# Performance work log

Measured on AMD Instinct MI355X. Metric: run time of the kernel, lower is better.

Reference implementation:

```python
import jax, jax.numpy as jnp
import numpy as np

B, N, D_IN, H, R = 4096, 32, 256, 256, 3
VIRTUAL_DECAY = 0.7


def setup_inputs() -> dict:
    key = jax.random.key(0)
    ks = jax.random.split(key, 16)
    def xavier(k, shape):
        fan_in, fan_out = shape[-1], shape[-2]
        lim = np.sqrt(6.0 / (fan_in + fan_out))
        return jax.random.uniform(k, shape, jnp.float32, -lim, lim)
    return {
        'input_vec': jax.random.normal(ks[0], (B, D_IN), jnp.float32),
        'child_h': jax.random.normal(ks[1], (B, N, H), jnp.float32),
        'child_c': jax.random.normal(ks[2], (B, N, H), jnp.float32),
        'relation_ids': jax.random.randint(ks[3], (B, N), 0, R, jnp.int32),
        'virtual_mask': jax.random.randint(ks[4], (B, N), 0, 2, jnp.int32).astype(bool),
        'rel_emb': xavier(ks[5], (R, H)),
        'W_i': xavier(ks[6], (H, D_IN + H)), 'b_i': jnp.full((H,), 0.1, jnp.float32),
        'W_f': xavier(ks[7], (R, H, H)),     'b_f': jnp.full((R, H), 0.1, jnp.float32),
        'W_o': xavier(ks[8], (H, D_IN + H)), 'b_o': jnp.full((H,), 0.1, jnp.float32),
        'W_u': xavier(ks[9], (H, D_IN + H)), 'b_u': jnp.full((H,), 0.1, jnp.float32),
        'w_att': xavier(ks[10], (1, H)).reshape(H), 'b_att': jnp.full((1,), 0.1, jnp.float32),
    }


def reference(input_vec, child_h, child_c, relation_ids, virtual_mask,
              rel_emb, W_i, b_i, W_f, b_f, W_o, b_o, W_u, b_u, w_att, b_att):
    # virtual-node decay applied to both child states
    decay = jnp.where(virtual_mask, VIRTUAL_DECAY, 1.0)[..., None]          # (B,N,1)
    ch = child_h * decay                                                     # (B,N,H)
    cc = child_c * decay                                                     # (B,N,H)

    # relation-aware attention over children (softmax over child axis)
    re = rel_emb[relation_ids]                                               # (B,N,H)
    scores = jnp.einsum('bnh,h->bn', re + ch, w_att) + b_att[0]              # (B,N)
    attn = jax.nn.softmax(scores, axis=1)[..., None]                         # (B,N,1)
    child_h_sum = jnp.sum(ch * attn, axis=1)                                 # (B,H)

    # relation-routed forget gates: compute all R linears, gather by relation id
    # NOTE: original applies NO sigmoid to f (faithful to source)
    f_all = jnp.einsum('bnh,rgh->bnrg', ch, W_f) + b_f                       # (B,N,R,H)
    f = jnp.take_along_axis(f_all, relation_ids[:, :, None, None], axis=2)[:, :, 0, :]  # (B,N,H)
    child_c_sum = jnp.sum(f * cc, axis=1)                                    # (B,H)

    combined = jnp.concatenate([input_vec, child_h_sum], axis=-1)            # (B,D_IN+H)
    i = jax.nn.sigmoid(combined @ W_i.T + b_i)
    o = jax.nn.sigmoid(combined @ W_o.T + b_o)
    u = jnp.tanh(combined @ W_u.T + b_u)
    c = i * u + child_c_sum
    h = o * jnp.tanh(c)
    return (h, c)
```

## Files before the change

### kernel.cpp

```cpp
#include <hip/hip_runtime.h>
#include <hip/hip_bf16.h>
#include <math.h>


#define B_    4096
#define N_    32
#define H_    256
#define DIN_  256
#define R_    3
#define MB    8
#define NBC   2
#define CHUNKS (MB / NBC)
#define DECAY 0.7f

#define WS_WF   0
#define WS_WI   196608
#define WS_WO   327680
#define WS_WU   458752
#define WS_ELEMS 589824

typedef __bf16 bf16;
typedef bf16  bf16x8 __attribute__((ext_vector_type(8)));
typedef float f32x4  __attribute__((ext_vector_type(4)));

__device__ __forceinline__ float sigmoidf_(float x) { return 1.0f / (1.0f + __expf(-x)); }

__device__ __forceinline__ bf16x8 cvt8_nt(const float* p) {
    f32x4 a = __builtin_nontemporal_load((const f32x4*)p);
    f32x4 b = __builtin_nontemporal_load((const f32x4*)(p + 4));
    bf16x8 r;
    #pragma unroll
    for (int j = 0; j < 4; ++j) { r[j] = (bf16)a[j]; r[j + 4] = (bf16)b[j]; }
    return r;
}
__device__ __forceinline__ bf16x8 cvt8_c(const float* p) {
    f32x4 a = *(const f32x4*)p;
    f32x4 b = *(const f32x4*)(p + 4);
    bf16x8 r;
    #pragma unroll
    for (int j = 0; j < 4; ++j) { r[j] = (bf16)a[j]; r[j + 4] = (bf16)b[j]; }
    return r;
}

template<bool WSW>
__device__ __forceinline__ bf16x8 ldw8(const bf16* wsp, const float* fp, int idx) {
    if constexpr (WSW) return *(const bf16x8*)(wsp + idx);
    else               return cvt8_c(fp + idx);
}

__global__ __launch_bounds__(256) void wprep(
    const float* __restrict__ Wf, const float* __restrict__ Wi,
    const float* __restrict__ Wo, const float* __restrict__ Wu,
    bf16* __restrict__ ws)
{
    int i = (blockIdx.x * 256 + threadIdx.x) * 8;
    const float* src; int off;
    if      (i < WS_WI) { src = Wf; off = i - WS_WF; }
    else if (i < WS_WO) { src = Wi; off = i - WS_WI; }
    else if (i < WS_WU) { src = Wo; off = i - WS_WO; }
    else                { src = Wu; off = i - WS_WU; }
    *(bf16x8*)(ws + i) = cvt8_c(src + off);
}

template<bool WSW>
__global__ __launch_bounds__(512) __attribute__((amdgpu_waves_per_eu(4, 4)))
void fused_main(
    const float* __restrict__ ivec,
    const float* __restrict__ child_h, const float* __restrict__ child_c,
    const int*  __restrict__ rel_ids,  const void* __restrict__ vmaskp,
    const float* __restrict__ rel_emb,
    const float* __restrict__ W_i, const float* __restrict__ b_i,
    const float* __restrict__ W_f, const float* __restrict__ b_f,
    const float* __restrict__ W_o, const float* __restrict__ b_o,
    const float* __restrict__ W_u, const float* __restrict__ b_u,
    const float* __restrict__ w_att, const float* __restrict__ b_att,
    const bf16* __restrict__ ws, float* __restrict__ out)
{
    __shared__ __align__(16) bf16 chs[NBC][N_][264];
    __shared__ __align__(16) bf16 hsumL[MB][264];
    __shared__ float csL[MB][H_];
    __shared__ float watt[H_];
    __shared__ float bfl[R_][H_];
    __shared__ float dall[MB][N_];
    __shared__ int   rids[MB][N_];
    __shared__ float scoreT[NBC * N_];
    __shared__ float rdotL[4];
    __shared__ int   m8flag;

    const int tid  = threadIdx.x;
    const int wave = tid >> 6;
    const int lane = tid & 63;
    const int t    = lane & 15;
    const int q    = lane >> 4;
    const int b0   = blockIdx.x * MB;

    const bf16* wfb = ws + WS_WF;
    const bf16* wib = ws + WS_WI;
    const bf16* wob = ws + WS_WO;
    const bf16* wub = ws + WS_WU;

    if (tid < 64) {
        const unsigned char* vb = (const unsigned char*)vmaskp;
        int bad = vb[tid * 4 + 1] | vb[tid * 4 + 2] | vb[tid * 4 + 3];
        unsigned long long any = __ballot(bad != 0);
        if (tid == 0) m8flag = (any != 0ull) ? 1 : 0;
    }
    __syncthreads();

    if (tid < 256) {
        watt[tid] = w_att[tid];
        int idx = b0 * N_ + tid;
        rids[tid >> 5][tid & 31] = rel_ids[idx];
        bool vm = m8flag ? (((const unsigned char*)vmaskp)[idx] != 0)
                         : (((const int*)vmaskp)[idx] != 0);
        dall[tid >> 5][tid & 31] = vm ? DECAY : 1.0f;
    }
    for (int i = tid; i < R_ * H_; i += 512) ((float*)bfl)[i] = b_f[i];
    if (tid == 0) rdotL[3] = b_att[0];
    __syncthreads();

    if (wave < R_) {
        int r = wave;
        float p = 0.f;
        #pragma unroll
        for (int j = 0; j < 4; ++j) {
            int h = lane * 4 + j;
            p += rel_emb[r * H_ + h] * watt[h];
        }
        #pragma unroll
        for (int off = 32; off >= 1; off >>= 1) p += __shfl_xor(p, off);
        if (lane == 0) rdotL[r] = p;
    }

    for (int ck = 0; ck < CHUNKS; ++ck) {
        __syncthreads();

        {
            size_t base = (size_t)(b0 + ck * NBC) * (N_ * H_);
            float dp[4];
            #pragma unroll
            for (int it = 0; it < 4; ++it) {
                int ge = (it * 512 + tid) << 3;
                int row = ge >> 8;
                int h = ge & 255;
                f32x4 a = __builtin_nontemporal_load((const f32x4*)(child_h + base + ge));
                f32x4 b = __builtin_nontemporal_load((const f32x4*)(child_h + base + ge + 4));
                bf16x8 r; float p = 0.f;
                #pragma unroll
                for (int j = 0; j < 4; ++j) {
                    r[j] = (bf16)a[j]; r[j + 4] = (bf16)b[j];
                    p += a[j] * watt[h + j] + b[j] * watt[h + 4 + j];
                }
                *(bf16x8*)(&chs[row >> 5][row & 31][h]) = r;
                dp[it] = p;
            }
            #pragma unroll
            for (int off = 16; off >= 1; off >>= 1) {
                dp[0] += __shfl_xor(dp[0], off);
                dp[1] += __shfl_xor(dp[1], off);
                dp[2] += __shfl_xor(dp[2], off);
                dp[3] += __shfl_xor(dp[3], off);
            }
            if ((tid & 31) == 0) {
                int grp = tid >> 5;
                #pragma unroll
                for (int it = 0; it < 4; ++it) scoreT[it * 16 + grp] = dp[it];
            }
        }
        __syncthreads();

        float att;
        {
            int bi = lane >> 5, n = lane & 31;
            int bl = ck * NBC + bi;
            float d = dall[bl][n];
            float s = d * scoreT[lane] + rdotL[rids[bl][n]] + rdotL[3];
            float m = s;
            #pragma unroll
            for (int off = 16; off >= 1; off >>= 1) m = fmaxf(m, __shfl_xor(m, off));
            float e = __expf(s - m);
            float sum = e;
            #pragma unroll
            for (int off = 16; off >= 1; off >>= 1) sum += __shfl_xor(sum, off);
            att = (e / sum) * d;
        }

        {
            int bi = tid >> 8, g = tid & 255;
            int bl = ck * NBC + bi;
            float s = 0.f;
            #pragma unroll 8
            for (int n = 0; n < N_; ++n) {
                float av = __shfl(att, (bi << 5) | n);
                s += av * (float)chs[bi][n][g];
            }
            hsumL[bl][g] = (bf16)s;
        }

        f32x4 acc[2][4];
        #pragma unroll
        for (int i = 0; i < 2; ++i)
            #pragma unroll
            for (int j = 0; j < 4; ++j)
                #pragma unroll
                for (int c = 0; c < 4; ++c) acc[i][j][c] = 0.0f;

        bf16x8 bzero;
        #pragma unroll
        for (int i = 0; i < 8; ++i) bzero[i] = (bf16)0.0f;

        int myrid[4];
        #pragma unroll
        for (int nt = 0; nt < 4; ++nt)
            myrid[nt] = rids[ck * NBC + (nt >> 1)][((nt & 1) << 4) + t];

        #pragma unroll
        for (int kc = 0; kc < 8; ++kc) {
            const int k = kc * 32 + q * 8;
            bf16x8 v[4];
            #pragma unroll
            for (int nt = 0; nt < 4; ++nt)
                v[nt] = *(const bf16x8*)(&chs[nt >> 1][((nt & 1) << 4) + t][k]);
            #pragma unroll
            for (int r = 0; r < R_; ++r) {
                bf16x8 afrag[2];
                #pragma unroll
                for (int m2 = 0; m2 < 2; ++m2) {
                    int g = (wave * 2 + m2) * 16 + t;
                    afrag[m2] = ldw8<WSW>(wfb, W_f, (r * H_ + g) * H_ + k);
                }
                #pragma unroll
                for (int nt = 0; nt < 4; ++nt) {
                    bf16x8 vm = (myrid[nt] == r) ? v[nt] : bzero;
                    acc[0][nt] = __builtin_amdgcn_mfma_f32_16x16x32_bf16(afrag[0], vm, acc[0][nt], 0, 0, 0);
                    acc[1][nt] = __builtin_amdgcn_mfma_f32_16x16x32_bf16(afrag[1], vm, acc[1][nt], 0, 0, 0);
                }
            }
        }

        {
            f32x4 cc[2][2][2];
            #pragma unroll
            for (int m2 = 0; m2 < 2; ++m2)
                #pragma unroll
                for (int bi = 0; bi < NBC; ++bi) {
                    size_t cbase = (size_t)(b0 + ck * NBC + bi) * (N_ * H_);
                    #pragma unroll
                    for (int j = 0; j < 2; ++j)
                        cc[m2][bi][j] = __builtin_nontemporal_load(
                            (const f32x4*)(child_c + cbase + (size_t)(((j << 4) + t)) * H_
                                           + (wave * 2 + m2) * 16 + q * 4));
                }
            #pragma unroll
            for (int m2 = 0; m2 < 2; ++m2) {
                #pragma unroll
                for (int reg = 0; reg < 4; ++reg) {
                    const int g = (wave * 2 + m2) * 16 + q * 4 + reg;
                    #pragma unroll
                    for (int bi = 0; bi < NBC; ++bi) {
                        int bl = ck * NBC + bi;
                        float p = 0.f;
                        #pragma unroll
                        for (int j = 0; j < 2; ++j) {
                            int nt = bi * 2 + j;
                            int n  = (j << 4) + t;
                            float d = dall[bl][n];
                            p += cc[m2][bi][j][reg] * d
                                 * fmaf(d, acc[m2][nt][reg], bfl[rids[bl][n]][g]);
                        }
                        p += __shfl_xor(p, 1);
                        p += __shfl_xor(p, 2);
                        p += __shfl_xor(p, 4);
                        p += __shfl_xor(p, 8);
                        if (t == 0) csL[bl][g] = p;
                    }
                }
            }
        }
    }
    __syncthreads();

    const int j0 = wave * 32;
    const int tt = t & 7;
    f32x4 accI[2], accO[2], accU[2];
    #pragma unroll
    for (int c = 0; c < 2; ++c)
        #pragma unroll
        for (int r = 0; r < 4; ++r) { accI[c][r] = 0.f; accO[c][r] = 0.f; accU[c][r] = 0.f; }

    #pragma unroll
    for (int kc = 0; kc < 16; ++kc) {
        const int k = kc * 32 + q * 8;
        bf16x8 a;
        if (kc < 8) a = cvt8_nt(ivec + (size_t)(b0 + tt) * DIN_ + k);
        else        a = *(const bf16x8*)(&hsumL[tt][k - 256]);
        #pragma unroll
        for (int c = 0; c < 2; ++c) {
            int j = j0 + c * 16 + t;
            bf16x8 bI = ldw8<WSW>(wib, W_i, j * 512 + k);
            bf16x8 bO = ldw8<WSW>(wob, W_o, j * 512 + k);
            bf16x8 bU = ldw8<WSW>(wub, W_u, j * 512 + k);
            accI[c] = __builtin_amdgcn_mfma_f32_16x16x32_bf16(a, bI, accI[c], 0, 0, 0);
            accO[c] = __builtin_amdgcn_mfma_f32_16x16x32_bf16(a, bO, accO[c], 0, 0, 0);
            accU[c] = __builtin_amdgcn_mfma_f32_16x16x32_bf16(a, bU, accU[c], 0, 0, 0);
        }
    }

    if (q < 2) {
        #pragma unroll
        for (int c = 0; c < 2; ++c) {
            const int j = j0 + c * 16 + t;
            float biv = b_i[j], bov = b_o[j], buv = b_u[j];
            #pragma unroll
            for (int reg = 0; reg < 4; ++reg) {
                int bl = q * 4 + reg;
                size_t o1 = (size_t)(b0 + bl) * H_ + j;
                size_t o2 = (size_t)B_ * H_ + o1;
                float iv = sigmoidf_(accI[c][reg] + biv);
                float ov = sigmoidf_(accO[c][reg] + bov);
                float uv = tanhf(accU[c][reg] + buv);
                float cv = fmaf(iv, uv, csL[bl][j]);
                float hv = ov * tanhf(cv);
                __builtin_nontemporal_store(hv, out + o1);
                __builtin_nontemporal_store(cv, out + o2);
            }
        }
    }
}

extern "C" void kernel_launch(void* const* d_in, const int* in_sizes, int n_in,
                              void* d_out, int out_size, void* d_ws, size_t ws_size,
                              hipStream_t stream)
{
    const float* ivec    = (const float*)d_in[0];
    const float* child_h = (const float*)d_in[1];
    const float* child_c = (const float*)d_in[2];
    const int*   relids  = (const int*)d_in[3];
    const void*  vmask   = d_in[4];
    const float* rel_emb = (const float*)d_in[5];
    const float* W_i     = (const float*)d_in[6];
    const float* b_i     = (const float*)d_in[7];
    const float* W_f     = (const float*)d_in[8];
    const float* b_f     = (const float*)d_in[9];
    const float* W_o     = (const float*)d_in[10];
    const float* b_o     = (const float*)d_in[11];
    const float* W_u     = (const float*)d_in[12];
    const float* b_u     = (const float*)d_in[13];
    const float* w_att   = (const float*)d_in[14];
    const float* b_att   = (const float*)d_in[15];
    float* out = (float*)d_out;
    bf16*  ws  = (bf16*)d_ws;

    const bool wsw = (ws_size >= (size_t)WS_ELEMS * sizeof(bf16));

    if (wsw) {
        hipLaunchKernelGGL(wprep, dim3(WS_ELEMS / 8 / 256), dim3(256), 0, stream,
                           W_f, W_i, W_o, W_u, ws);
        hipLaunchKernelGGL((fused_main<true>), dim3(B_ / MB), dim3(512), 0, stream,
                           ivec, child_h, child_c, relids, vmask, rel_emb,
                           W_i, b_i, W_f, b_f, W_o, b_o, W_u, b_u, w_att, b_att,
                           ws, out);
    } else {
        hipLaunchKernelGGL((fused_main<false>), dim3(B_ / MB), dim3(512), 0, stream,
                           ivec, child_h, child_c, relids, vmask, rel_emb,
                           W_i, b_i, W_f, b_f, W_o, b_o, W_u, b_u, w_att, b_att,
                           ws, out);
    }
}
```

Before: 463.0 us.

## Double-buffer child_h chunks and double batch rows per block

Prefetches the next chunk's child_h into registers while the current chunk's attention and forget-gate MFMAs run, using a double-buffered LDS tile and score array. It also issues the child_c loads earlier, before the MFMA loop. MB goes from 8 to 16 so the final gate GEMM fills the full 16-row MFMA tile and the weights are reused across twice the rows. Occupancy hint drops to 2 waves per EU to make room for more registers and LDS, at the cost of fewer resident blocks and half as many blocks in the grid.

Result: no change. 466.1 us (+0.7%).

```diff
diff --git a/kernel.cpp b/kernel.cpp
--- a/kernel.cpp
+++ b/kernel.cpp
@@ -8,7 +8,7 @@
 #define H_    256
 #define DIN_  256
 #define R_    3
-#define MB    8
+#define MB    16
 #define NBC   2
 #define CHUNKS (MB / NBC)
 #define DECAY 0.7f
@@ -63,7 +63,7 @@
 }
 
 template<bool WSW>
-__global__ __launch_bounds__(512) __attribute__((amdgpu_waves_per_eu(4, 4)))
+__global__ __launch_bounds__(512) __attribute__((amdgpu_waves_per_eu(2, 2)))
 void fused_main(
     const float* __restrict__ ivec,
     const float* __restrict__ child_h, const float* __restrict__ child_c,
@@ -76,14 +76,14 @@
     const float* __restrict__ w_att, const float* __restrict__ b_att,
     const bf16* __restrict__ ws, float* __restrict__ out)
 {
-    __shared__ __align__(16) bf16 chs[NBC][N_][264];
+    __shared__ __align__(16) bf16 chs[2][NBC][N_][264];
     __shared__ __align__(16) bf16 hsumL[MB][264];
     __shared__ float csL[MB][H_];
     __shared__ float watt[H_];
     __shared__ float bfl[R_][H_];
     __shared__ float dall[MB][N_];
     __shared__ int   rids[MB][N_];
-    __shared__ float scoreT[NBC * N_];
+    __shared__ float scoreS[2][NBC * N_];
     __shared__ float rdotL[4];
     __shared__ int   m8flag;
 
@@ -107,8 +107,8 @@
     }
     __syncthreads();
 
-    if (tid < 256) {
-        watt[tid] = w_att[tid];
+    if (tid < H_) watt[tid] = w_att[tid];
+    {
         int idx = b0 * N_ + tid;
         rids[tid >> 5][tid & 31] = rel_ids[idx];
         bool vm = m8flag ? (((const unsigned char*)vmaskp)[idx] != 0)
@@ -132,49 +132,59 @@
         if (lane == 0) rdotL[r] = p;
     }
 
+    {
+        size_t base = (size_t)b0 * (N_ * H_);
+        float dp[4];
+        #pragma unroll
+        for (int it = 0; it < 4; ++it) {
+            int ge = (it * 512 + tid) << 3;
+            int row = ge >> 8, h = ge & 255;
+            f32x4 a = __builtin_nontemporal_load((const f32x4*)(child_h + base + ge));
+            f32x4 b = __builtin_nontemporal_load((const f32x4*)(child_h + base + ge + 4));
+            bf16x8 r; float p = 0.f;
+            #pragma unroll
+            for (int j = 0; j < 4; ++j) {
+                r[j] = (bf16)a[j]; r[j + 4] = (bf16)b[j];
+                p += a[j] * watt[h + j] + b[j] * watt[h + 4 + j];
+            }
+            *(bf16x8*)(&chs[0][row >> 5][row & 31][h]) = r;
+            dp[it] = p;
+        }
+        #pragma unroll
+        for (int off = 16; off >= 1; off >>= 1) {
+            dp[0] += __shfl_xor(dp[0], off);
+            dp[1] += __shfl_xor(dp[1], off);
+            dp[2] += __shfl_xor(dp[2], off);
+            dp[3] += __shfl_xor(dp[3], off);
+        }
+        if ((tid & 31) == 0) {
+            int grp = tid >> 5;
+            #pragma unroll
+            for (int it = 0; it < 4; ++it) scoreS[0][it * 16 + grp] = dp[it];
+        }
+    }
+    __syncthreads();
+
     for (int ck = 0; ck < CHUNKS; ++ck) {
-        __syncthreads();
-
-        {
-            size_t base = (size_t)(b0 + ck * NBC) * (N_ * H_);
-            float dp[4];
+        const int cur = ck & 1, nxt = cur ^ 1;
+
+        f32x4 hA[4], hB[4];
+        if (ck + 1 < CHUNKS) {
+            size_t base = (size_t)(b0 + (ck + 1) * NBC) * (N_ * H_);
             #pragma unroll
             for (int it = 0; it < 4; ++it) {
                 int ge = (it * 512 + tid) << 3;
-                int row = ge >> 8;
-                int h = ge & 255;
-                f32x4 a = __builtin_nontemporal_load((const f32x4*)(child_h + base + ge));
-                f32x4 b = __builtin_nontemporal_load((const f32x4*)(child_h + base + ge + 4));
-                bf16x8 r; float p = 0.f;
-                #pragma unroll
-                for (int j = 0; j < 4; ++j) {
-                    r[j] = (bf16)a[j]; r[j + 4] = (bf16)b[j];
-                    p += a[j] * watt[h + j] + b[j] * watt[h + 4 + j];
-                }
-                *(bf16x8*)(&chs[row >> 5][row & 31][h]) = r;
-                dp[it] = p;
-            }
-            #pragma unroll
-            for (int off = 16; off >= 1; off >>= 1) {
-                dp[0] += __shfl_xor(dp[0], off);
-                dp[1] += __shfl_xor(dp[1], off);
-                dp[2] += __shfl_xor(dp[2], off);
-                dp[3] += __shfl_xor(dp[3], off);
-            }
-            if ((tid & 31) == 0) {
-                int grp = tid >> 5;
-                #pragma unroll
-                for (int it = 0; it < 4; ++it) scoreT[it * 16 + grp] = dp[it];
-            }
-        }
-        __syncthreads();
+                hA[it] = __builtin_nontemporal_load((const f32x4*)(child_h + base + ge));
+                hB[it] = __builtin_nontemporal_load((const f32x4*)(child_h + base + ge + 4));
+            }
+        }
 
         float att;
         {
             int bi = lane >> 5, n = lane & 31;
             int bl = ck * NBC + bi;
             float d = dall[bl][n];
-            float s = d * scoreT[lane] + rdotL[rids[bl][n]] + rdotL[3];
+            float s = d * scoreS[cur][lane] + rdotL[rids[bl][n]] + rdotL[3];
             float m = s;
             #pragma unroll
             for (int off = 16; off >= 1; off >>= 1) m = fmaxf(m, __shfl_xor(m, off));
@@ -184,6 +194,19 @@
             for (int off = 16; off >= 1; off >>= 1) sum += __shfl_xor(sum, off);
             att = (e / sum) * d;
         }
+
+        f32x4 cc[2][2][2];
+        #pragma unroll
+        for (int m2 = 0; m2 < 2; ++m2)
+            #pragma unroll
+            for (int bi = 0; bi < NBC; ++bi) {
+                size_t cbase = (size_t)(b0 + ck * NBC + bi) * (N_ * H_);
+                #pragma unroll
+                for (int j = 0; j < 2; ++j)
+                    cc[m2][bi][j] = __builtin_nontemporal_load(
+                        (const f32x4*)(child_c + cbase + (size_t)(((j << 4) + t)) * H_
+                                       + (wave * 2 + m2) * 16 + q * 4));
+            }
 
         {
             int bi = tid >> 8, g = tid & 255;
@@ -192,7 +215,7 @@
             #pragma unroll 8
             for (int n = 0; n < N_; ++n) {
                 float av = __shfl(att, (bi << 5) | n);
-                s += av * (float)chs[bi][n][g];
+                s += av * (float)chs[cur][bi][n][g];
             }
             hsumL[bl][g] = (bf16)s;
         }
@@ -220,7 +243,7 @@
             bf16x8 v[4];
             #pragma unroll
             for (int nt = 0; nt < 4; ++nt)
-                v[nt] = *(const bf16x8*)(&chs[nt >> 1][((nt & 1) << 4) + t][k]);
+                v[nt] = *(const bf16x8*)(&chs[cur][nt >> 1][((nt & 1) << 4) + t][k]);
             #pragma unroll
             for (int r = 0; r < R_; ++r) {
                 bf16x8 afrag[2];
@@ -238,50 +261,64 @@
             }
         }
 
-        {
-            f32x4 cc[2][2][2];
-            #pragma unroll
-            for (int m2 = 0; m2 < 2; ++m2)
+        #pragma unroll
+        for (int m2 = 0; m2 < 2; ++m2) {
+            #pragma unroll
+            for (int reg = 0; reg < 4; ++reg) {
+                const int g = (wave * 2 + m2) * 16 + q * 4 + reg;
                 #pragma unroll
                 for (int bi = 0; bi < NBC; ++bi) {
-                    size_t cbase = (size_t)(b0 + ck * NBC + bi) * (N_ * H_);
+                    int bl = ck * NBC + bi;
+                    float p = 0.f;
                     #pragma unroll
-                    for (int j = 0; j < 2; ++j)
-                        cc[m2][bi][j] = __builtin_nontemporal_load(
-                            (const f32x4*)(child_c + cbase + (size_t)(((j << 4) + t)) * H_
-                                           + (wave * 2 + m2) * 16 + q * 4));
+                    for (int j = 0; j < 2; ++j) {
+                        int nt = bi * 2 + j;
+                        int n  = (j << 4) + t;
+                        float d = dall[bl][n];
+                        p += cc[m2][bi][j][reg] * d
+                             * fmaf(d, acc[m2][nt][reg], bfl[rids[bl][n]][g]);
+                    }
+                    p += __shfl_xor(p, 1);
+                    p += __shfl_xor(p, 2);
+                    p += __shfl_xor(p, 4);
+                    p += __shfl_xor(p, 8);
+                    if (t == 0) csL[bl][g] = p;
                 }
-            #pragma unroll
-            for (int m2 = 0; m2 < 2; ++m2) {
-                #pragma unroll
-                for (int reg = 0; reg < 4; ++reg) {
-                    const int g = (wave * 2 + m2) * 16 + q * 4 + reg;
-                    #pragma unroll
-                    for (int bi = 0; bi < NBC; ++bi) {
-                        int bl = ck * NBC + bi;
-                        float p = 0.f;
-                        #pragma unroll
-                        for (int j = 0; j < 2; ++j) {
-                            int nt = bi * 2 + j;
-                            int n  = (j << 4) + t;
-                            float d = dall[bl][n];
-                            p += cc[m2][bi][j][reg] * d
-                                 * fmaf(d, acc[m2][nt][reg], bfl[rids[bl][n]][g]);
-                        }
-                        p += __shfl_xor(p, 1);
-                        p += __shfl_xor(p, 2);
-                        p += __shfl_xor(p, 4);
-                        p += __shfl_xor(p, 8);
-                        if (t == 0) csL[bl][g] = p;
-                    }
+            }
+        }
+
+        if (ck + 1 < CHUNKS) {
+            float dp[4];
+            #pragma unroll
+            for (int it = 0; it < 4; ++it) {
+                int ge = (it * 512 + tid) << 3;
+                int row = ge >> 8, h = ge & 255;
+                bf16x8 r; float p = 0.f;
+                #pragma unroll
+                for (int j = 0; j < 4; ++j) {
+                    r[j] = (bf16)hA[it][j]; r[j + 4] = (bf16)hB[it][j];
+                    p += hA[it][j] * watt[h + j] + hB[it][j] * watt[h + 4 + j];
                 }
-            }
-        }
-    }
-    __syncthreads();
+                *(bf16x8*)(&chs[nxt][row >> 5][row & 31][h]) = r;
+                dp[it] = p;
+            }
+            #pragma unroll
+            for (int off = 16; off >= 1; off >>= 1) {
+                dp[0] += __shfl_xor(dp[0], off);
+                dp[1] += __shfl_xor(dp[1], off);
+                dp[2] += __shfl_xor(dp[2], off);
+                dp[3] += __shfl_xor(dp[3], off);
+            }
+            if ((tid & 31) == 0) {
+                int grp = tid >> 5;
+                #pragma unroll
+                for (int it = 0; it < 4; ++it) scoreS[nxt][it * 16 + grp] = dp[it];
+            }
+        }
+        __syncthreads();
+    }
 
     const int j0 = wave * 32;
-    const int tt = t & 7;
     f32x4 accI[2], accO[2], accU[2];
     #pragma unroll
     for (int c = 0; c < 2; ++c)
@@ -292,8 +329,8 @@
     for (int kc = 0; kc < 16; ++kc) {
         const int k = kc * 32 + q * 8;
         bf16x8 a;
-        if (kc < 8) a = cvt8_nt(ivec + (size_t)(b0 + tt) * DIN_ + k);
-        else        a = *(const bf16x8*)(&hsumL[tt][k - 256]);
+        if (kc < 8) a = cvt8_nt(ivec + (size_t)(b0 + t) * DIN_ + k);
+        else        a = *(const bf16x8*)(&hsumL[t][k - 256]);
         #pragma unroll
         for (int c = 0; c < 2; ++c) {
             int j = j0 + c * 16 + t;
@@ -306,24 +343,22 @@
         }
     }
 
-    if (q < 2) {
-        #pragma unroll
-        for (int c = 0; c < 2; ++c) {
-            const int j = j0 + c * 16 + t;
-            float biv = b_i[j], bov = b_o[j], buv = b_u[j];
-            #pragma unroll
-            for (int reg = 0; reg < 4; ++reg) {
-                int bl = q * 4 + reg;
-                size_t o1 = (size_t)(b0 + bl) * H_ + j;
-                size_t o2 = (size_t)B_ * H_ + o1;
-                float iv = sigmoidf_(accI[c][reg] + biv);
-                float ov = sigmoidf_(accO[c][reg] + bov);
-                float uv = tanhf(accU[c][reg] + buv);
-                float cv = fmaf(iv, uv, csL[bl][j]);
-                float hv = ov * tanhf(cv);
-                __builtin_nontemporal_store(hv, out + o1);
-                __builtin_nontemporal_store(cv, out + o2);
-            }
+    #pragma unroll
+    for (int c = 0; c < 2; ++c) {
+        const int j = j0 + c * 16 + t;
+        float biv = b_i[j], bov = b_o[j], buv = b_u[j];
+        #pragma unroll
+        for (int reg = 0; reg < 4; ++reg) {
+            int bl = q * 4 + reg;
+            size_t o1 = (size_t)(b0 + bl) * H_ + j;
+            size_t o2 = (size_t)B_ * H_ + o1;
+            float iv = sigmoidf_(accI[c][reg] + biv);
+            float ov = sigmoidf_(accO[c][reg] + bov);
+            float uv = tanhf(accU[c][reg] + buv);
+            float cv = fmaf(iv, uv, csL[bl][j]);
+            float hv = ov * tanhf(cv);
+            __builtin_nontemporal_store(hv, out + o1);
+            __builtin_nontemporal_store(cv, out + o2);
         }
     }
 }
```

## Double batch rows per block to amortize weight fragment loads across more MFMAs

Applied to the files above, without the earlier changes.

Each block now handles 16 batch rows instead of 8, and each chunk covers 4 rows instead of 2. Every W_f fragment and every W_i/W_o/W_u fragment therefore feeds twice as many MFMA columns, and the final gate GEMM fills all 16 rows of the MFMA tile rather than duplicating 8. The cost is more registers and LDS per block: the accumulator arrays double and occupancy is lowered to 2 waves per EU. The grid also shrinks to 256 blocks, which may leave some compute units underused.

Result: faster. 424.9 us (-8.2%).

```diff
diff --git a/kernel.cpp b/kernel.cpp
--- a/kernel.cpp
+++ b/kernel.cpp
@@ -8,8 +8,8 @@
 #define H_    256
 #define DIN_  256
 #define R_    3
-#define MB    8
-#define NBC   2
+#define MB    16
+#define NBC   4
 #define CHUNKS (MB / NBC)
 #define DECAY 0.7f
 
@@ -63,7 +63,7 @@
 }
 
 template<bool WSW>
-__global__ __launch_bounds__(512) __attribute__((amdgpu_waves_per_eu(4, 4)))
+__global__ __launch_bounds__(512) __attribute__((amdgpu_waves_per_eu(2, 2)))
 void fused_main(
     const float* __restrict__ ivec,
     const float* __restrict__ child_h, const float* __restrict__ child_c,
@@ -107,8 +107,8 @@
     }
     __syncthreads();
 
-    if (tid < 256) {
-        watt[tid] = w_att[tid];
+    if (tid < H_) watt[tid] = w_att[tid];
+    {
         int idx = b0 * N_ + tid;
         rids[tid >> 5][tid & 31] = rel_ids[idx];
         bool vm = m8flag ? (((const unsigned char*)vmaskp)[idx] != 0)
@@ -137,9 +137,9 @@
 
         {
             size_t base = (size_t)(b0 + ck * NBC) * (N_ * H_);
-            float dp[4];
-            #pragma unroll
-            for (int it = 0; it < 4; ++it) {
+            float dp[8];
+            #pragma unroll
+            for (int it = 0; it < 8; ++it) {
                 int ge = (it * 512 + tid) << 3;
                 int row = ge >> 8;
                 int h = ge & 255;
@@ -156,52 +156,61 @@
             }
             #pragma unroll
             for (int off = 16; off >= 1; off >>= 1) {
-                dp[0] += __shfl_xor(dp[0], off);
-                dp[1] += __shfl_xor(dp[1], off);
-                dp[2] += __shfl_xor(dp[2], off);
-                dp[3] += __shfl_xor(dp[3], off);
+                #pragma unroll
+                for (int it = 0; it < 8; ++it) dp[it] += __shfl_xor(dp[it], off);
             }
             if ((tid & 31) == 0) {
                 int grp = tid >> 5;
                 #pragma unroll
-                for (int it = 0; it < 4; ++it) scoreT[it * 16 + grp] = dp[it];
+                for (int it = 0; it < 8; ++it) scoreT[it * 16 + grp] = dp[it];
             }
         }
         __syncthreads();
 
-        float att;
+        float att0, att1;
         {
-            int bi = lane >> 5, n = lane & 31;
-            int bl = ck * NBC + bi;
-            float d = dall[bl][n];
-            float s = d * scoreT[lane] + rdotL[rids[bl][n]] + rdotL[3];
-            float m = s;
-            #pragma unroll
-            for (int off = 16; off >= 1; off >>= 1) m = fmaxf(m, __shfl_xor(m, off));
-            float e = __expf(s - m);
-            float sum = e;
-            #pragma unroll
-            for (int off = 16; off >= 1; off >>= 1) sum += __shfl_xor(sum, off);
-            att = (e / sum) * d;
-        }
-
-        {
-            int bi = tid >> 8, g = tid & 255;
+            int n  = lane & 31;
+            int bi = lane >> 5;
+            int bl0 = ck * NBC + bi, bl1 = bl0 + 2;
+            float d0 = dall[bl0][n], d1 = dall[bl1][n];
+            float s0 = d0 * scoreT[lane]      + rdotL[rids[bl0][n]] + rdotL[3];
+            float s1 = d1 * scoreT[64 + lane] + rdotL[rids[bl1][n]] + rdotL[3];
+            float m0 = s0, m1 = s1;
+            #pragma unroll
+            for (int off = 16; off >= 1; off >>= 1) {
+                m0 = fmaxf(m0, __shfl_xor(m0, off));
+                m1 = fmaxf(m1, __shfl_xor(m1, off));
+            }
+            float e0 = __expf(s0 - m0), e1 = __expf(s1 - m1);
+            float u0 = e0, u1 = e1;
+            #pragma unroll
+            for (int off = 16; off >= 1; off >>= 1) {
+                u0 += __shfl_xor(u0, off);
+                u1 += __shfl_xor(u1, off);
+            }
+            att0 = (e0 / u0) * d0;
+            att1 = (e1 / u1) * d1;
+        }
+
+        #pragma unroll
+        for (int ps = 0; ps < 2; ++ps) {
+            int bi = (tid >> 8) + ps * 2;
+            int g  = tid & 255;
             int bl = ck * NBC + bi;
             float s = 0.f;
             #pragma unroll 8
             for (int n = 0; n < N_; ++n) {
-                float av = __shfl(att, (bi << 5) | n);
+                float av = __shfl(ps ? att1 : att0, ((tid >> 8) << 5) | n);
                 s += av * (float)chs[bi][n][g];
             }
             hsumL[bl][g] = (bf16)s;
         }
 
-        f32x4 acc[2][4];
+        f32x4 acc[2][8];
         #pragma unroll
         for (int i = 0; i < 2; ++i)
             #pragma unroll
-            for (int j = 0; j < 4; ++j)
+            for (int j = 0; j < 8; ++j)
                 #pragma unroll
                 for (int c = 0; c < 4; ++c) acc[i][j][c] = 0.0f;
 
@@ -209,17 +218,17 @@
         #pragma unroll
         for (int i = 0; i < 8; ++i) bzero[i] = (bf16)0.0f;
 
-        int myrid[4];
-        #pragma unroll
-        for (int nt = 0; nt < 4; ++nt)
+        int myrid[8];
+        #pragma unroll
+        for (int nt = 0; nt < 8; ++nt)
             myrid[nt] = rids[ck * NBC + (nt >> 1)][((nt & 1) << 4) + t];
 
         #pragma unroll
         for (int kc = 0; kc < 8; ++kc) {
             const int k = kc * 32 + q * 8;
-            bf16x8 v[4];
-            #pragma unroll
-            for (int nt = 0; nt < 4; ++nt)
+            bf16x8 v[8];
+            #pragma unroll
+            for (int nt = 0; nt < 8; ++nt)
                 v[nt] = *(const bf16x8*)(&chs[nt >> 1][((nt & 1) << 4) + t][k]);
             #pragma unroll
             for (int r = 0; r < R_; ++r) {
@@ -230,7 +239,7 @@
                     afrag[m2] = ldw8<WSW>(wfb, W_f, (r * H_ + g) * H_ + k);
                 }
                 #pragma unroll
-                for (int nt = 0; nt < 4; ++nt) {
+                for (int nt = 0; nt < 8; ++nt) {
                     bf16x8 vm = (myrid[nt] == r) ? v[nt] : bzero;
                     acc[0][nt] = __builtin_amdgcn_mfma_f32_16x16x32_bf16(afrag[0], vm, acc[0][nt], 0, 0, 0);
                     acc[1][nt] = __builtin_amdgcn_mfma_f32_16x16x32_bf16(afrag[1], vm, acc[1][nt], 0, 0, 0);
@@ -239,7 +248,7 @@
         }
 
         {
-            f32x4 cc[2][2][2];
+            f32x4 cc[2][4][2];
             #pragma unroll
             for (int m2 = 0; m2 < 2; ++m2)
                 #pragma unroll
@@ -281,7 +290,6 @@
     __syncthreads();
 
     const int j0 = wave * 32;
-    const int tt = t & 7;
     f32x4 accI[2], accO[2], accU[2];
     #pragma unroll
     for (int c = 0; c < 2; ++c)
@@ -292,8 +300,8 @@
     for (int kc = 0; kc < 16; ++kc) {
         const int k = kc * 32 + q * 8;
         bf16x8 a;
-        if (kc < 8) a = cvt8_nt(ivec + (size_t)(b0 + tt) * DIN_ + k);
-        else        a = *(const bf16x8*)(&hsumL[tt][k - 256]);
+        if (kc < 8) a = cvt8_nt(ivec + (size_t)(b0 + t) * DIN_ + k);
+        else        a = *(const bf16x8*)(&hsumL[t][k - 256]);
         #pragma unroll
         for (int c = 0; c < 2; ++c) {
             int j = j0 + c * 16 + t;
@@ -306,24 +314,22 @@
         }
     }
 
-    if (q < 2) {
-        #pragma unroll
-        for (int c = 0; c < 2; ++c) {
-            const int j = j0 + c * 16 + t;
-            float biv = b_i[j], bov = b_o[j], buv = b_u[j];
-            #pragma unroll
-            for (int reg = 0; reg < 4; ++reg) {
-                int bl = q * 4 + reg;
-                size_t o1 = (size_t)(b0 + bl) * H_ + j;
-                size_t o2 = (size_t)B_ * H_ + o1;
-                float iv = sigmoidf_(accI[c][reg] + biv);
-                float ov = sigmoidf_(accO[c][reg] + bov);
-                float uv = tanhf(accU[c][reg] + buv);
-                float cv = fmaf(iv, uv, csL[bl][j]);
-                float hv = ov * tanhf(cv);
-                __builtin_nontemporal_store(hv, out + o1);
-                __builtin_nontemporal_store(cv, out + o2);
-            }
+    #pragma unroll
+    for (int c = 0; c < 2; ++c) {
+        const int j = j0 + c * 16 + t;
+        float biv = b_i[j], bov = b_o[j], buv = b_u[j];
+        #pragma unroll
+        for (int reg = 0; reg < 4; ++reg) {
+            int bl = q * 4 + reg;
+            size_t o1 = (size_t)(b0 + bl) * H_ + j;
+            size_t o2 = (size_t)B_ * H_ + o1;
+            float iv = sigmoidf_(accI[c][reg] + biv);
+            float ov = sigmoidf_(accO[c][reg] + bov);
+            float uv = tanhf(accU[c][reg] + buv);
+            float cv = fmaf(iv, uv, csL[bl][j]);
+            float hv = ov * tanhf(cv);
+            __builtin_nontemporal_store(hv, out + o1);
+            __builtin_nontemporal_store(cv, out + o2);
         }
     }
 }
```

## Double batch rows per block and spill child_c_sum through output buffer

Applied to the files above, without the earlier changes.

Raises batch rows per block from 8 to 16 and processes 8 batches per chunk, so each W_f fragment load feeds 16 MFMA column tiles instead of 4 and the gate GEMM fills all 16 MFMA rows. The shared csL array is removed; child_c_sum is written to the c half of the output and read back in the epilogue, which frees LDS but adds a global round trip. Occupancy is lowered to 2 waves per EU to make room for the larger accumulator arrays (acc[2][16], v[16]), which risks less latency hiding.

After: 422.6 us. 1.1x faster.

```diff
diff --git a/kernel.cpp b/kernel.cpp
--- a/kernel.cpp
+++ b/kernel.cpp
@@ -8,8 +8,8 @@
 #define H_    256
 #define DIN_  256
 #define R_    3
-#define MB    8
-#define NBC   2
+#define MB    16
+#define NBC   8
 #define CHUNKS (MB / NBC)
 #define DECAY 0.7f
 
@@ -63,7 +63,7 @@
 }
 
 template<bool WSW>
-__global__ __launch_bounds__(512) __attribute__((amdgpu_waves_per_eu(4, 4)))
+__global__ __launch_bounds__(512) __attribute__((amdgpu_waves_per_eu(2, 2)))
 void fused_main(
     const float* __restrict__ ivec,
     const float* __restrict__ child_h, const float* __restrict__ child_c,
@@ -78,7 +78,6 @@
 {
     __shared__ __align__(16) bf16 chs[NBC][N_][264];
     __shared__ __align__(16) bf16 hsumL[MB][264];
-    __shared__ float csL[MB][H_];
     __shared__ float watt[H_];
     __shared__ float bfl[R_][H_];
     __shared__ float dall[MB][N_];
@@ -107,8 +106,8 @@
     }
     __syncthreads();
 
-    if (tid < 256) {
-        watt[tid] = w_att[tid];
+    if (tid < H_) watt[tid] = w_att[tid];
+    {
         int idx = b0 * N_ + tid;
         rids[tid >> 5][tid & 31] = rel_ids[idx];
         bool vm = m8flag ? (((const unsigned char*)vmaskp)[idx] != 0)
@@ -137,9 +136,9 @@
 
         {
             size_t base = (size_t)(b0 + ck * NBC) * (N_ * H_);
-            float dp[4];
-            #pragma unroll
-            for (int it = 0; it < 4; ++it) {
+            float dp[16];
+            #pragma unroll
+            for (int it = 0; it < 16; ++it) {
                 int ge = (it * 512 + tid) << 3;
                 int row = ge >> 8;
                 int h = ge & 255;
@@ -156,52 +155,58 @@
             }
             #pragma unroll
             for (int off = 16; off >= 1; off >>= 1) {
-                dp[0] += __shfl_xor(dp[0], off);
-                dp[1] += __shfl_xor(dp[1], off);
-                dp[2] += __shfl_xor(dp[2], off);
-                dp[3] += __shfl_xor(dp[3], off);
+                #pragma unroll
+                for (int it = 0; it < 16; ++it) dp[it] += __shfl_xor(dp[it], off);
             }
             if ((tid & 31) == 0) {
                 int grp = tid >> 5;
                 #pragma unroll
-                for (int it = 0; it < 4; ++it) scoreT[it * 16 + grp] = dp[it];
+                for (int it = 0; it < 16; ++it) scoreT[it * 16 + grp] = dp[it];
             }
         }
         __syncthreads();
 
-        float att;
+        float att[4];
         {
-            int bi = lane >> 5, n = lane & 31;
-            int bl = ck * NBC + bi;
-            float d = dall[bl][n];
-            float s = d * scoreT[lane] + rdotL[rids[bl][n]] + rdotL[3];
-            float m = s;
-            #pragma unroll
-            for (int off = 16; off >= 1; off >>= 1) m = fmaxf(m, __shfl_xor(m, off));
-            float e = __expf(s - m);
-            float sum = e;
-            #pragma unroll
-            for (int off = 16; off >= 1; off >>= 1) sum += __shfl_xor(sum, off);
-            att = (e / sum) * d;
-        }
-
-        {
-            int bi = tid >> 8, g = tid & 255;
+            int n  = lane & 31;
+            int hb = lane >> 5;
+            #pragma unroll
+            for (int k = 0; k < 4; ++k) {
+                int bi = 2 * k + hb;
+                int bl = ck * NBC + bi;
+                float d = dall[bl][n];
+                float s = d * scoreT[64 * k + lane] + rdotL[rids[bl][n]] + rdotL[3];
+                float m = s;
+                #pragma unroll
+                for (int off = 16; off >= 1; off >>= 1) m = fmaxf(m, __shfl_xor(m, off));
+                float e = __expf(s - m);
+                float sum = e;
+                #pragma unroll
+                for (int off = 16; off >= 1; off >>= 1) sum += __shfl_xor(sum, off);
+                att[k] = (e / sum) * d;
+            }
+        }
+
+        #pragma unroll
+        for (int ps = 0; ps < 4; ++ps) {
+            int hb = tid >> 8;
+            int bi = 2 * ps + hb;
+            int g  = tid & 255;
             int bl = ck * NBC + bi;
             float s = 0.f;
             #pragma unroll 8
             for (int n = 0; n < N_; ++n) {
-                float av = __shfl(att, (bi << 5) | n);
+                float av = __shfl(att[ps], n + (hb << 5));
                 s += av * (float)chs[bi][n][g];
             }
             hsumL[bl][g] = (bf16)s;
         }
 
-        f32x4 acc[2][4];
+        f32x4 acc[2][16];
         #pragma unroll
         for (int i = 0; i < 2; ++i)
             #pragma unroll
-            for (int j = 0; j < 4; ++j)
+            for (int j = 0; j < 16; ++j)
                 #pragma unroll
                 for (int c = 0; c < 4; ++c) acc[i][j][c] = 0.0f;
 
@@ -209,17 +214,17 @@
         #pragma unroll
         for (int i = 0; i < 8; ++i) bzero[i] = (bf16)0.0f;
 
-        int myrid[4];
-        #pragma unroll
-        for (int nt = 0; nt < 4; ++nt)
+        int myrid[16];
+        #pragma unroll
+        for (int nt = 0; nt < 16; ++nt)
             myrid[nt] = rids[ck * NBC + (nt >> 1)][((nt & 1) << 4) + t];
 
         #pragma unroll
         for (int kc = 0; kc < 8; ++kc) {
             const int k = kc * 32 + q * 8;
-            bf16x8 v[4];
-            #pragma unroll
-            for (int nt = 0; nt < 4; ++nt)
+            bf16x8 v[16];
+            #pragma unroll
+            for (int nt = 0; nt < 16; ++nt)
                 v[nt] = *(const bf16x8*)(&chs[nt >> 1][((nt & 1) << 4) + t][k]);
             #pragma unroll
             for (int r = 0; r < R_; ++r) {
@@ -230,7 +235,7 @@
                     afrag[m2] = ldw8<WSW>(wfb, W_f, (r * H_ + g) * H_ + k);
                 }
                 #pragma unroll
-                for (int nt = 0; nt < 4; ++nt) {
+                for (int nt = 0; nt < 16; ++nt) {
                     bf16x8 vm = (myrid[nt] == r) ? v[nt] : bzero;
                     acc[0][nt] = __builtin_amdgcn_mfma_f32_16x16x32_bf16(afrag[0], vm, acc[0][nt], 0, 0, 0);
                     acc[1][nt] = __builtin_amdgcn_mfma_f32_16x16x32_bf16(afrag[1], vm, acc[1][nt], 0, 0, 0);
@@ -238,16 +243,18 @@
             }
         }
 
-        {
+        #pragma unroll
+        for (int bg = 0; bg < 4; ++bg) {
             f32x4 cc[2][2][2];
             #pragma unroll
             for (int m2 = 0; m2 < 2; ++m2)
                 #pragma unroll
-                for (int bi = 0; bi < NBC; ++bi) {
+                for (int bp = 0; bp < 2; ++bp) {
+                    int bi = bg * 2 + bp;
                     size_t cbase = (size_t)(b0 + ck * NBC + bi) * (N_ * H_);
                     #pragma unroll
                     for (int j = 0; j < 2; ++j)
-                        cc[m2][bi][j] = __builtin_nontemporal_load(
+                        cc[m2][bp][j] = __builtin_nontemporal_load(
                             (const f32x4*)(child_c + cbase + (size_t)(((j << 4) + t)) * H_
                                            + (wave * 2 + m2) * 16 + q * 4));
                 }
@@ -257,7 +264,8 @@
                 for (int reg = 0; reg < 4; ++reg) {
                     const int g = (wave * 2 + m2) * 16 + q * 4 + reg;
                     #pragma unroll
-                    for (int bi = 0; bi < NBC; ++bi) {
+                    for (int bp = 0; bp < 2; ++bp) {
+                        int bi = bg * 2 + bp;
                         int bl = ck * NBC + bi;
                         float p = 0.f;
                         #pragma unroll
@@ -265,14 +273,15 @@
                             int nt = bi * 2 + j;
                             int n  = (j << 4) + t;
                             float d = dall[bl][n];
-                            p += cc[m2][bi][j][reg] * d
+                            p += cc[m2][bp][j][reg] * d
                                  * fmaf(d, acc[m2][nt][reg], bfl[rids[bl][n]][g]);
                         }
                         p += __shfl_xor(p, 1);
                         p += __shfl_xor(p, 2);
                         p += __shfl_xor(p, 4);
                         p += __shfl_xor(p, 8);
-                        if (t == 0) csL[bl][g] = p;
+                        if (t == 0)
+                            out[(size_t)B_ * H_ + (size_t)(b0 + bl) * H_ + g] = p;
                     }
                 }
             }
@@ -281,7 +290,6 @@
     __syncthreads();
 
     const int j0 = wave * 32;
-    const int tt = t & 7;
     f32x4 accI[2], accO[2], accU[2];
     #pragma unroll
     for (int c = 0; c < 2; ++c)
@@ -292,8 +300,8 @@
     for (int kc = 0; kc < 16; ++kc) {
         const int k = kc * 32 + q * 8;
         bf16x8 a;
-        if (kc < 8) a = cvt8_nt(ivec + (size_t)(b0 + tt) * DIN_ + k);
-        else        a = *(const bf16x8*)(&hsumL[tt][k - 256]);
+        if (kc < 8) a = cvt8_nt(ivec + (size_t)(b0 + t) * DIN_ + k);
+        else        a = *(const bf16x8*)(&hsumL[t][k - 256]);
         #pragma unroll
         for (int c = 0; c < 2; ++c) {
             int j = j0 + c * 16 + t;
@@ -306,24 +314,23 @@
         }
     }
 
-    if (q < 2) {
-        #pragma unroll
-        for (int c = 0; c < 2; ++c) {
-            const int j = j0 + c * 16 + t;
-            float biv = b_i[j], bov = b_o[j], buv = b_u[j];
-            #pragma unroll
-            for (int reg = 0; reg < 4; ++reg) {
-                int bl = q * 4 + reg;
-                size_t o1 = (size_t)(b0 + bl) * H_ + j;
-                size_t o2 = (size_t)B_ * H_ + o1;
-                float iv = sigmoidf_(accI[c][reg] + biv);
-                float ov = sigmoidf_(accO[c][reg] + bov);
-                float uv = tanhf(accU[c][reg] + buv);
-                float cv = fmaf(iv, uv, csL[bl][j]);
-                float hv = ov * tanhf(cv);
-                __builtin_nontemporal_store(hv, out + o1);
-                __builtin_nontemporal_store(cv, out + o2);
-            }
+    #pragma unroll
+    for (int c = 0; c < 2; ++c) {
+        const int j = j0 + c * 16 + t;
+        float biv = b_i[j], bov = b_o[j], buv = b_u[j];
+        #pragma unroll
+        for (int reg = 0; reg < 4; ++reg) {
+            int bl = q * 4 + reg;
+            size_t o1 = (size_t)(b0 + bl) * H_ + j;
+            size_t o2 = (size_t)B_ * H_ + o1;
+            float csv = out[o2];
+            float iv = sigmoidf_(accI[c][reg] + biv);
+            float ov = sigmoidf_(accO[c][reg] + bov);
+            float uv = tanhf(accU[c][reg] + buv);
+            float cv = fmaf(iv, uv, csv);
+            float hv = ov * tanhf(cv);
+            __builtin_nontemporal_store(hv, out + o1);
+            __builtin_nontemporal_store(cv, out + o2);
         }
     }
 }
```
